# Kernel tuning notes

Measured on AMD Instinct MI355X. Metric: run time of the kernel, lower is better.

Reference implementation:

```python
import jax, jax.numpy as jnp
import numpy as np

INF = 10000000000.0
D_KEY = 512
SCALE = np.sqrt(D_KEY).astype(np.float32)

def setup_inputs() -> dict:
    key = jax.random.key(0)
    kq, kk, kv = jax.random.split(key, 3)
    B, S, D = 16, 2048, D_KEY
    return {
        "query": jax.random.normal(kq, (B, S, D), dtype=jnp.float32),
        "key": jax.random.normal(kk, (B, S, D), dtype=jnp.float32),
        "value": jax.random.normal(kv, (B, S, D), dtype=jnp.float32),
    }

def reference(query, key, value):
    # dot_products = Q @ K^T, shape [B, S, S]
    scores = jnp.einsum('bqd,bkd->bqk', query, key)
    S = key.shape[1]
    # causal mask: subtract INF on strict upper triangle (applied BEFORE scaling,
    # matching the original which subtracts tri*INF then divides by scale)
    tri = jnp.triu(jnp.ones((S, S), dtype=scores.dtype), k=1) * INF
    scores = scores - tri[None, :, :]
    attn = jax.nn.softmax(scores / SCALE, axis=-1)
    return jnp.einsum('bqk,bkd->bqd', attn, value)
```

## Files before the change

### kernel.cpp

```cpp
#include <hip/hip_runtime.h>

typedef float  f32x4 __attribute__((ext_vector_type(4)));
typedef short  s16x8 __attribute__((ext_vector_type(8)));
typedef short  s16x4 __attribute__((ext_vector_type(4)));

#define B_   16
#define S_   2048
#define D_   512
#define BM   32
#define BN   256
#define KPF  8
#define RL   0.06375872112626925f

__device__ __forceinline__ short f2bf(float f){
    unsigned u = __float_as_uint(f);
    u += 0x7fffu + ((u >> 16) & 1u);
    return (short)(u >> 16);
}

__device__ __forceinline__ f32x4 shfl_xor4(f32x4 v, int mask){
    f32x4 r; r[0]=__shfl_xor(v[0],mask); r[1]=__shfl_xor(v[1],mask);
             r[2]=__shfl_xor(v[2],mask); r[3]=__shfl_xor(v[3],mask); return r;
}

__global__ void cast_k_kernel(const float* __restrict__ k, short* __restrict__ kb){
    const long n4 = (long)B_*S_*D_/4;
    const float4* src = (const float4*)k;
    for (long t = (long)blockIdx.x*blockDim.x + threadIdx.x; t < n4;
         t += (long)gridDim.x*blockDim.x){
        float4 v = src[t];
        s16x4 o; o[0]=f2bf(v.x); o[1]=f2bf(v.y); o[2]=f2bf(v.z); o[3]=f2bf(v.w);
        *(s16x4*)(kb + t*4) = o;
    }
}

__global__ void transpose_v_kernel(const float* __restrict__ v, short* __restrict__ vt){
    __shared__ float tile[64][65];
    int b  = blockIdx.z;
    int s0 = blockIdx.x * 64;
    int d0 = blockIdx.y * 64;
    int t  = threadIdx.x;
    int r  = t >> 2;
    int c4 = (t & 3) * 16;
    const float* src = v + ((long)b*S_ + s0 + r)*D_ + d0 + c4;
    float4 a0 = ((const float4*)src)[0];
    float4 a1 = ((const float4*)src)[1];
    float4 a2 = ((const float4*)src)[2];
    float4 a3 = ((const float4*)src)[3];
    tile[r][c4+ 0]=a0.x; tile[r][c4+ 1]=a0.y; tile[r][c4+ 2]=a0.z; tile[r][c4+ 3]=a0.w;
    tile[r][c4+ 4]=a1.x; tile[r][c4+ 5]=a1.y; tile[r][c4+ 6]=a1.z; tile[r][c4+ 7]=a1.w;
    tile[r][c4+ 8]=a2.x; tile[r][c4+ 9]=a2.y; tile[r][c4+10]=a2.z; tile[r][c4+11]=a2.w;
    tile[r][c4+12]=a3.x; tile[r][c4+13]=a3.y; tile[r][c4+14]=a3.z; tile[r][c4+15]=a3.w;
    __syncthreads();
    s16x8 w0, w1;
    #pragma unroll
    for (int i = 0; i < 8; ++i)  w0[i] = f2bf(tile[c4+i][r]);
    #pragma unroll
    for (int i = 0; i < 8; ++i)  w1[i] = f2bf(tile[c4+8+i][r]);
    short* dst = vt + ((long)b*D_ + d0 + r)*S_ + s0 + c4;
    *(s16x8*)dst       = w0;
    *(s16x8*)(dst + 8) = w1;
}

__global__ __launch_bounds__(512, 2) void flash_kernel(
    const float* __restrict__ q, const short* __restrict__ kb,
    const short* __restrict__ vt, float* __restrict__ out)
{
    __shared__ __align__(16) short q_lds[BM*D_];
    __shared__ __align__(16) short p_lds[2][BM*BN];
    __shared__ float lred[BM][8];

    int bx = blockIdx.x;
    int lo = bx & 7;
    int hi = bx >> 3;
    int batch = 2*lo + (hi & 1);
    int t = hi >> 1;
    int qt = (t < 32) ? (63 - t) : (t - 32);
    int q0 = qt * BM;

    int tid  = threadIdx.x;
    int w    = tid >> 6;
    int lane = tid & 63;
    int m    = lane & 15;
    int quad = lane >> 4;

    {
        int r  = tid >> 4;
        int cb = (tid & 15) << 5;
        const float* qrow = q + ((long)batch*S_ + q0 + r)*D_;
        #pragma unroll
        for (int gi = 0; gi < 4; ++gi){
            int c = cb + gi*8;
            float4 f0 = *(const float4*)(qrow + c);
            float4 f1 = *(const float4*)(qrow + c + 4);
            s16x8 vv;
            vv[0]=f2bf(f0.x); vv[1]=f2bf(f0.y); vv[2]=f2bf(f0.z); vv[3]=f2bf(f0.w);
            vv[4]=f2bf(f1.x); vv[5]=f2bf(f1.y); vv[6]=f2bf(f1.z); vv[7]=f2bf(f1.w);
            int g = c >> 3;
            *(s16x8*)&q_lds[r*D_ + (((g ^ (r & 7)) & 63) << 3)] = vv;
        }
    }
    __syncthreads();

    f32x4 o_acc[2][4];
    #pragma unroll
    for (int a = 0; a < 2; ++a)
        #pragma unroll
        for (int b2 = 0; b2 < 4; ++b2) o_acc[a][b2] = (f32x4)0.0f;
    f32x4 cs[2];
    cs[0] = (f32x4)0.0f; cs[1] = (f32x4)0.0f;

    const short* kbb = kb + (long)batch*S_*D_;
    const short* vtb = vt + (long)batch*D_*S_;
    int jmax = (q0 + BM - 1) >> 8;

    s16x8 kr0[KPF], kr1[KPF];
    {
        const short* kp = kbb + ((long)(w*32 + m))*D_ + quad*8;
        #pragma unroll
        for (int pf = 0; pf < KPF; ++pf){
            kr0[pf] = *(const s16x8*)(kp + pf*32);
            kr1[pf] = *(const s16x8*)(kp + pf*32 + 16*D_);
        }
    }

    for (int j = 0; j <= jmax; ++j){
        int kbase = j << 8;
        const short* kp0 = kbb + ((long)(kbase + w*32 + m))*D_ + quad*8;

        const short* vp0 = vtb + ((long)(w*64 + m))*S_ + kbase + quad*8;
        s16x8 vA[4], vB[4];
        #pragma unroll
        for (int g = 0; g < 4; ++g) vA[g] = *(const s16x8*)(vp0 + g*16*S_);
        #pragma unroll
        for (int g = 0; g < 4; ++g) vB[g] = *(const s16x8*)(vp0 + 32 + g*16*S_);

        f32x4 acc[2][2];
        acc[0][0]=(f32x4)0.0f; acc[0][1]=(f32x4)0.0f;
        acc[1][0]=(f32x4)0.0f; acc[1][1]=(f32x4)0.0f;
        __builtin_amdgcn_s_setprio(1);
        #pragma unroll
        for (int ks = 0; ks < 16; ++ks){
            const int sl = ks & (KPF - 1);
            s16x8 b0 = kr0[sl];
            s16x8 b1 = kr1[sl];
            if (ks + KPF < 16){
                const short* kp = kp0 + (ks + KPF)*32;
                kr0[sl] = *(const s16x8*)kp;
                kr1[sl] = *(const s16x8*)(kp + 16*D_);
            }
            int gq = ((ks*4 + quad) ^ (m & 7)) << 3;
            s16x8 a0 = *(const s16x8*)&q_lds[ m      *D_ + gq];
            s16x8 a1 = *(const s16x8*)&q_lds[(16 + m)*D_ + gq];
            acc[0][0] = __builtin_amdgcn_mfma_f32_16x16x32_bf16(a0, b0, acc[0][0], 0,0,0);
            acc[0][1] = __builtin_amdgcn_mfma_f32_16x16x32_bf16(a0, b1, acc[0][1], 0,0,0);
            acc[1][0] = __builtin_amdgcn_mfma_f32_16x16x32_bf16(a1, b0, acc[1][0], 0,0,0);
            acc[1][1] = __builtin_amdgcn_mfma_f32_16x16x32_bf16(a1, b1, acc[1][1], 0,0,0);
        }
        __builtin_amdgcn_s_setprio(0);

        short* pl = p_lds[j & 1];
        if (j == jmax){
            #pragma unroll
            for (int mt = 0; mt < 2; ++mt)
                #pragma unroll
                for (int nt = 0; nt < 2; ++nt){
                    int col = w*32 + nt*16 + m;
                    int kg  = kbase + col;
                    int g   = col >> 3;
                    #pragma unroll
                    for (int rr = 0; rr < 4; ++rr){
                        int row = mt*16 + quad*4 + rr;
                        int qg  = q0 + row;
                        float p = (kg > qg) ? 0.0f : exp2f(acc[mt][nt][rr] * RL);
                        cs[mt][rr] += p;
                        pl[row*BN + (((g ^ (row & 7)) & 31) << 3) + (col & 7)] = f2bf(p);
                    }
                }
        } else {
            #pragma unroll
            for (int mt = 0; mt < 2; ++mt)
                #pragma unroll
                for (int nt = 0; nt < 2; ++nt){
                    int col = w*32 + nt*16 + m;
                    int g   = col >> 3;
                    #pragma unroll
                    for (int rr = 0; rr < 4; ++rr){
                        int row = mt*16 + quad*4 + rr;
                        float p = exp2f(acc[mt][nt][rr] * RL);
                        cs[mt][rr] += p;
                        pl[row*BN + (((g ^ (row & 7)) & 31) << 3) + (col & 7)] = f2bf(p);
                    }
                }
        }

        __syncthreads();

        if (j < jmax){
            const short* kp = kbb + ((long)(kbase + 256 + w*32 + m))*D_ + quad*8;
            #pragma unroll
            for (int pf = 0; pf < KPF; ++pf){
                kr0[pf] = *(const s16x8*)(kp + pf*32);
                kr1[pf] = *(const s16x8*)(kp + pf*32 + 16*D_);
            }
        }

        const short* plr = p_lds[j & 1];
        __builtin_amdgcn_s_setprio(1);
        #pragma unroll
        for (int ks = 0; ks < 8; ++ks){
            s16x8 vb0, vb1, vb2, vb3;
            if (ks & 1){ vb0=vB[0]; vb1=vB[1]; vb2=vB[2]; vb3=vB[3]; }
            else       { vb0=vA[0]; vb1=vA[1]; vb2=vA[2]; vb3=vA[3]; }
            if (ks + 2 < 8){
                const short* vp = vp0 + (ks+2)*32;
                if (ks & 1){
                    #pragma unroll
                    for (int g = 0; g < 4; ++g) vB[g] = *(const s16x8*)(vp + g*16*S_);
                } else {
                    #pragma unroll
                    for (int g = 0; g < 4; ++g) vA[g] = *(const s16x8*)(vp + g*16*S_);
                }
            }
            int gp = ((ks*4 + quad) ^ (m & 7)) << 3;
            s16x8 pa0 = *(const s16x8*)&plr[ m      *BN + gp];
            s16x8 pa1 = *(const s16x8*)&plr[(16 + m)*BN + gp];
            o_acc[0][0] = __builtin_amdgcn_mfma_f32_16x16x32_bf16(pa0, vb0, o_acc[0][0], 0,0,0);
            o_acc[0][1] = __builtin_amdgcn_mfma_f32_16x16x32_bf16(pa0, vb1, o_acc[0][1], 0,0,0);
            o_acc[0][2] = __builtin_amdgcn_mfma_f32_16x16x32_bf16(pa0, vb2, o_acc[0][2], 0,0,0);
            o_acc[0][3] = __builtin_amdgcn_mfma_f32_16x16x32_bf16(pa0, vb3, o_acc[0][3], 0,0,0);
            o_acc[1][0] = __builtin_amdgcn_mfma_f32_16x16x32_bf16(pa1, vb0, o_acc[1][0], 0,0,0);
            o_acc[1][1] = __builtin_amdgcn_mfma_f32_16x16x32_bf16(pa1, vb1, o_acc[1][1], 0,0,0);
            o_acc[1][2] = __builtin_amdgcn_mfma_f32_16x16x32_bf16(pa1, vb2, o_acc[1][2], 0,0,0);
            o_acc[1][3] = __builtin_amdgcn_mfma_f32_16x16x32_bf16(pa1, vb3, o_acc[1][3], 0,0,0);
        }
        __builtin_amdgcn_s_setprio(0);
    }

    #pragma unroll
    for (int msk = 1; msk < 16; msk <<= 1){
        cs[0] = cs[0] + shfl_xor4(cs[0], msk);
        cs[1] = cs[1] + shfl_xor4(cs[1], msk);
    }
    if (m == 0){
        #pragma unroll
        for (int mt = 0; mt < 2; ++mt)
            #pragma unroll
            for (int rr = 0; rr < 4; ++rr)
                lred[mt*16 + quad*4 + rr][w] = cs[mt][rr];
    }
    __syncthreads();

    float* ob = out + ((long)batch*S_ + q0)*D_ + w*64;
    #pragma unroll
    for (int mt = 0; mt < 2; ++mt){
        f32x4 inv;
        #pragma unroll
        for (int rr = 0; rr < 4; ++rr){
            int row = mt*16 + quad*4 + rr;
            f32x4 p0 = *(const f32x4*)&lred[row][0];
            f32x4 p1 = *(const f32x4*)&lred[row][4];
            f32x4 sm = p0 + p1;
            inv[rr] = 1.0f / ((sm[0]+sm[1]) + (sm[2]+sm[3]));
        }
        #pragma unroll
        for (int nt = 0; nt < 4; ++nt){
            f32x4 vv = o_acc[mt][nt] * inv;
            #pragma unroll
            for (int rr = 0; rr < 4; ++rr)
                ob[(long)(mt*16 + quad*4 + rr)*D_ + nt*16 + m] = vv[rr];
        }
    }
}

extern "C" void kernel_launch(void* const* d_in, const int* in_sizes, int n_in,
                              void* d_out, int out_size, void* d_ws, size_t ws_size,
                              hipStream_t stream) {
    const float* q = (const float*)d_in[0];
    const float* k = (const float*)d_in[1];
    const float* v = (const float*)d_in[2];
    float* out = (float*)d_out;
    short* kbb = (short*)d_ws;
    short* vtb = kbb + (size_t)B_*S_*D_;
    cast_k_kernel<<<8192, 256, 0, stream>>>(k, kbb);
    transpose_v_kernel<<<dim3(S_/64, D_/64, B_), 256, 0, stream>>>(v, vtb);
    flash_kernel<<<1024, 512, 0, stream>>>(q, kbb, vtb, out);
}
```

Measured before the change: 508.5 us.

## Hand-schedule K/V global loads with inline asm and explicit vmcnt waits

Replaces compiler-scheduled K and V register prefetch with inline-asm global_load_dwordx4 and explicit s_waitcnt vmcnt counts. The K ring shrinks from 8 to 4 slots, V loads are issued after QK^T, and the next tile's K loads are issued right after the barrier so they overlap the PV MFMAs. It also drops the occupancy hint of 2 from launch_bounds and removes setprio. The aim is finer control of memory latency hiding and lower register pressure, at the cost of fragile hand-counted waits. On the last tile it issues K loads that are never used.

Measured after the change: 490.0 us. 1.04x faster.

```diff
diff --git a/kernel.cpp b/kernel.cpp
--- a/kernel.cpp
+++ b/kernel.cpp
@@ -9,7 +9,6 @@
 #define D_   512
 #define BM   32
 #define BN   256
-#define KPF  8
 #define RL   0.06375872112626925f
 
 __device__ __forceinline__ short f2bf(float f){
@@ -62,7 +61,55 @@
     *(s16x8*)(dst + 8) = w1;
 }
 
-__global__ __launch_bounds__(512, 2) void flash_kernel(
+
+#define GLOAD(dst, ptr) \
+    asm volatile("global_load_dwordx4 %0, %1, off" : "=&v"(dst) : "v"(ptr))
+
+#define WAITV(N) { \
+    asm volatile("s_waitcnt vmcnt(" #N ")" ::: "memory"); \
+    __builtin_amdgcn_sched_barrier(0); }
+
+#define QKSTEP(ks, WN) { \
+    WAITV(WN); \
+    int gq = (((ks)*4 + quad) ^ (m & 7)) << 3; \
+    s16x8 a0 = *(const s16x8*)&q_lds[ m      *D_ + gq]; \
+    s16x8 a1 = *(const s16x8*)&q_lds[(16 + m)*D_ + gq]; \
+    acc[0][0] = __builtin_amdgcn_mfma_f32_16x16x32_bf16(a0, kr0[(ks)&3], acc[0][0], 0,0,0); \
+    acc[0][1] = __builtin_amdgcn_mfma_f32_16x16x32_bf16(a0, kr1[(ks)&3], acc[0][1], 0,0,0); \
+    acc[1][0] = __builtin_amdgcn_mfma_f32_16x16x32_bf16(a1, kr0[(ks)&3], acc[1][0], 0,0,0); \
+    acc[1][1] = __builtin_amdgcn_mfma_f32_16x16x32_bf16(a1, kr1[(ks)&3], acc[1][1], 0,0,0); \
+    if ((ks) + 4 < 16){ \
+        GLOAD(kr0[(ks)&3], kp0 + ((ks)+4)*32); \
+        GLOAD(kr1[(ks)&3], kp0 + ((ks)+4)*32 + 16*D_); \
+    } }
+
+#define PVSTEP(ks, WN, VG) { \
+    WAITV(WN); \
+    int gp = (((ks)*4 + quad) ^ (m & 7)) << 3; \
+    s16x8 pa0 = *(const s16x8*)&plr[ m      *BN + gp]; \
+    s16x8 pa1 = *(const s16x8*)&plr[(16 + m)*BN + gp]; \
+    o_acc[0][0] = __builtin_amdgcn_mfma_f32_16x16x32_bf16(pa0, VG[0], o_acc[0][0],0,0,0); \
+    o_acc[0][1] = __builtin_amdgcn_mfma_f32_16x16x32_bf16(pa0, VG[1], o_acc[0][1],0,0,0); \
+    o_acc[0][2] = __builtin_amdgcn_mfma_f32_16x16x32_bf16(pa0, VG[2], o_acc[0][2],0,0,0); \
+    o_acc[0][3] = __builtin_amdgcn_mfma_f32_16x16x32_bf16(pa0, VG[3], o_acc[0][3],0,0,0); \
+    o_acc[1][0] = __builtin_amdgcn_mfma_f32_16x16x32_bf16(pa1, VG[0], o_acc[1][0],0,0,0); \
+    o_acc[1][1] = __builtin_amdgcn_mfma_f32_16x16x32_bf16(pa1, VG[1], o_acc[1][1],0,0,0); \
+    o_acc[1][2] = __builtin_amdgcn_mfma_f32_16x16x32_bf16(pa1, VG[2], o_acc[1][2],0,0,0); \
+    o_acc[1][3] = __builtin_amdgcn_mfma_f32_16x16x32_bf16(pa1, VG[3], o_acc[1][3],0,0,0); \
+    if ((ks) + 2 < 8){ \
+        GLOAD(VG[0], vp0 + ((ks)+2)*32 + 0*16*S_); \
+        GLOAD(VG[1], vp0 + ((ks)+2)*32 + 1*16*S_); \
+        GLOAD(VG[2], vp0 + ((ks)+2)*32 + 2*16*S_); \
+        GLOAD(VG[3], vp0 + ((ks)+2)*32 + 3*16*S_); \
+    } }
+
+#define ISSUE_KRING(KP) { \
+    GLOAD(kr0[0], (KP) + 0*32); GLOAD(kr1[0], (KP) + 0*32 + 16*D_); \
+    GLOAD(kr0[1], (KP) + 1*32); GLOAD(kr1[1], (KP) + 1*32 + 16*D_); \
+    GLOAD(kr0[2], (KP) + 2*32); GLOAD(kr1[2], (KP) + 2*32 + 16*D_); \
+    GLOAD(kr0[3], (KP) + 3*32); GLOAD(kr1[3], (KP) + 3*32 + 16*D_); }
+
+__global__ __launch_bounds__(512) void flash_kernel(
     const float* __restrict__ q, const short* __restrict__ kb,
     const short* __restrict__ vt, float* __restrict__ out)
 {
@@ -114,50 +161,31 @@
     const short* vtb = vt + (long)batch*D_*S_;
     int jmax = (q0 + BM - 1) >> 8;
 
-    s16x8 kr0[KPF], kr1[KPF];
+    s16x8 kr0[4], kr1[4];
+    s16x8 vA[4], vB[4];
+
     {
         const short* kp = kbb + ((long)(w*32 + m))*D_ + quad*8;
-        #pragma unroll
-        for (int pf = 0; pf < KPF; ++pf){
-            kr0[pf] = *(const s16x8*)(kp + pf*32);
-            kr1[pf] = *(const s16x8*)(kp + pf*32 + 16*D_);
-        }
+        ISSUE_KRING(kp);
     }
 
     for (int j = 0; j <= jmax; ++j){
         int kbase = j << 8;
         const short* kp0 = kbb + ((long)(kbase + w*32 + m))*D_ + quad*8;
-
         const short* vp0 = vtb + ((long)(w*64 + m))*S_ + kbase + quad*8;
-        s16x8 vA[4], vB[4];
-        #pragma unroll
-        for (int g = 0; g < 4; ++g) vA[g] = *(const s16x8*)(vp0 + g*16*S_);
-        #pragma unroll
-        for (int g = 0; g < 4; ++g) vB[g] = *(const s16x8*)(vp0 + 32 + g*16*S_);
 
         f32x4 acc[2][2];
         acc[0][0]=(f32x4)0.0f; acc[0][1]=(f32x4)0.0f;
         acc[1][0]=(f32x4)0.0f; acc[1][1]=(f32x4)0.0f;
-        __builtin_amdgcn_s_setprio(1);
-        #pragma unroll
-        for (int ks = 0; ks < 16; ++ks){
-            const int sl = ks & (KPF - 1);
-            s16x8 b0 = kr0[sl];
-            s16x8 b1 = kr1[sl];
-            if (ks + KPF < 16){
-                const short* kp = kp0 + (ks + KPF)*32;
-                kr0[sl] = *(const s16x8*)kp;
-                kr1[sl] = *(const s16x8*)(kp + 16*D_);
-            }
-            int gq = ((ks*4 + quad) ^ (m & 7)) << 3;
-            s16x8 a0 = *(const s16x8*)&q_lds[ m      *D_ + gq];
-            s16x8 a1 = *(const s16x8*)&q_lds[(16 + m)*D_ + gq];
-            acc[0][0] = __builtin_amdgcn_mfma_f32_16x16x32_bf16(a0, b0, acc[0][0], 0,0,0);
-            acc[0][1] = __builtin_amdgcn_mfma_f32_16x16x32_bf16(a0, b1, acc[0][1], 0,0,0);
-            acc[1][0] = __builtin_amdgcn_mfma_f32_16x16x32_bf16(a1, b0, acc[1][0], 0,0,0);
-            acc[1][1] = __builtin_amdgcn_mfma_f32_16x16x32_bf16(a1, b1, acc[1][1], 0,0,0);
-        }
-        __builtin_amdgcn_s_setprio(0);
+        QKSTEP( 0,6)  QKSTEP( 1,6)  QKSTEP( 2,6)  QKSTEP( 3,6)
+        QKSTEP( 4,6)  QKSTEP( 5,6)  QKSTEP( 6,6)  QKSTEP( 7,6)
+        QKSTEP( 8,6)  QKSTEP( 9,6)  QKSTEP(10,6)  QKSTEP(11,6)
+        QKSTEP(12,6)  QKSTEP(13,4)  QKSTEP(14,2)  QKSTEP(15,0)
+
+        GLOAD(vA[0], vp0 + 0*16*S_); GLOAD(vA[1], vp0 + 1*16*S_);
+        GLOAD(vA[2], vp0 + 2*16*S_); GLOAD(vA[3], vp0 + 3*16*S_);
+        GLOAD(vB[0], vp0 + 32 + 0*16*S_); GLOAD(vB[1], vp0 + 32 + 1*16*S_);
+        GLOAD(vB[2], vp0 + 32 + 2*16*S_); GLOAD(vB[3], vp0 + 32 + 3*16*S_);
 
         short* pl = p_lds[j & 1];
         if (j == jmax){
@@ -194,47 +222,19 @@
                 }
         }
 
-        __syncthreads();
-
-        if (j < jmax){
-            const short* kp = kbb + ((long)(kbase + 256 + w*32 + m))*D_ + quad*8;
-            #pragma unroll
-            for (int pf = 0; pf < KPF; ++pf){
-                kr0[pf] = *(const s16x8*)(kp + pf*32);
-                kr1[pf] = *(const s16x8*)(kp + pf*32 + 16*D_);
-            }
+        asm volatile("s_waitcnt lgkmcnt(0)" ::: "memory");
+        __builtin_amdgcn_sched_barrier(0);
+        __builtin_amdgcn_s_barrier();
+
+        {
+            long kbn = (j < jmax) ? (long)(kbase + 256) : 0;
+            const short* kpn = kbb + (kbn + (long)(w*32 + m))*D_ + quad*8;
+            ISSUE_KRING(kpn);
         }
 
         const short* plr = p_lds[j & 1];
-        __builtin_amdgcn_s_setprio(1);
-        #pragma unroll
-        for (int ks = 0; ks < 8; ++ks){
-            s16x8 vb0, vb1, vb2, vb3;
-            if (ks & 1){ vb0=vB[0]; vb1=vB[1]; vb2=vB[2]; vb3=vB[3]; }
-            else       { vb0=vA[0]; vb1=vA[1]; vb2=vA[2]; vb3=vA[3]; }
-            if (ks + 2 < 8){
-                const short* vp = vp0 + (ks+2)*32;
-                if (ks & 1){
-                    #pragma unroll
-                    for (int g = 0; g < 4; ++g) vB[g] = *(const s16x8*)(vp + g*16*S_);
-                } else {
-                    #pragma unroll
-                    for (int g = 0; g < 4; ++g) vA[g] = *(const s16x8*)(vp + g*16*S_);
-                }
-            }
-            int gp = ((ks*4 + quad) ^ (m & 7)) << 3;
-            s16x8 pa0 = *(const s16x8*)&plr[ m      *BN + gp];
-            s16x8 pa1 = *(const s16x8*)&plr[(16 + m)*BN + gp];
-            o_acc[0][0] = __builtin_amdgcn_mfma_f32_16x16x32_bf16(pa0, vb0, o_acc[0][0], 0,0,0);
-            o_acc[0][1] = __builtin_amdgcn_mfma_f32_16x16x32_bf16(pa0, vb1, o_acc[0][1], 0,0,0);
-            o_acc[0][2] = __builtin_amdgcn_mfma_f32_16x16x32_bf16(pa0, vb2, o_acc[0][2], 0,0,0);
-            o_acc[0][3] = __builtin_amdgcn_mfma_f32_16x16x32_bf16(pa0, vb3, o_acc[0][3], 0,0,0);
-            o_acc[1][0] = __builtin_amdgcn_mfma_f32_16x16x32_bf16(pa1, vb0, o_acc[1][0], 0,0,0);
-            o_acc[1][1] = __builtin_amdgcn_mfma_f32_16x16x32_bf16(pa1, vb1, o_acc[1][1], 0,0,0);
-            o_acc[1][2] = __builtin_amdgcn_mfma_f32_16x16x32_bf16(pa1, vb2, o_acc[1][2], 0,0,0);
-            o_acc[1][3] = __builtin_amdgcn_mfma_f32_16x16x32_bf16(pa1, vb3, o_acc[1][3], 0,0,0);
-        }
-        __builtin_amdgcn_s_setprio(0);
+        PVSTEP(0,12,vA)  PVSTEP(1,12,vB)  PVSTEP(2,4,vA)  PVSTEP(3,4,vB)
+        PVSTEP(4, 4,vA)  PVSTEP(5, 4,vB)  PVSTEP(6,4,vA)  PVSTEP(7,0,vB)
     }
 
     #pragma unroll
```
